# Kernel optimization log

Measured on AMD Instinct MI355X. Metric: run time of the kernel, lower is better.

The kernel has to match this reference:

```python
import jax, jax.numpy as jnp
import numpy as np

B, N, M, F, BF = 16, 1024, 12, 64, 128
N_CONV = 3
VOCAB = 100
BN_EPS = 1e-3  # keras BatchNormalization default epsilon


def _bn(x, gamma, beta):
    # inference-mode BN with moving_mean=0, moving_var=1 (keras defaults)
    return gamma * (x * (1.0 / jnp.sqrt(1.0 + BN_EPS))) + beta


def setup_inputs() -> dict:
    key = jax.random.key(0)
    ks = jax.random.split(key, 16)
    in_fea = 2 * F + BF
    inp = {
        'atom_types': jax.random.randint(ks[0], (B, N), 0, VOCAB, dtype=jnp.int32),
        'bond_fea': jax.random.normal(ks[1], (B, N, M, BF), dtype=jnp.float32),
        'nbr_list': jax.random.randint(ks[2], (B, N, M), 0, N, dtype=jnp.int32),
        'target_index': jax.random.randint(ks[3], (B, 64), 0, N, dtype=jnp.int32),
        'emb': jax.random.normal(ks[4], (VOCAB, F), dtype=jnp.float32) * 0.05,
        'core_w': jax.random.normal(ks[5], (N_CONV, in_fea, F), dtype=jnp.float32) / np.sqrt(in_fea),
        'core_b': jnp.zeros((N_CONV, F), dtype=jnp.float32),
        'filt_w': jax.random.normal(ks[6], (N_CONV, in_fea, 1), dtype=jnp.float32) / np.sqrt(in_fea),
        'filt_b': jnp.zeros((N_CONV, 1), dtype=jnp.float32),
        'bna_g': jnp.ones((N_CONV, F), dtype=jnp.float32),
        'bna_b': jnp.zeros((N_CONV, F), dtype=jnp.float32),
        'bnb_g': jnp.ones((N_CONV, F), dtype=jnp.float32),
        'bnb_b': jnp.zeros((N_CONV, F), dtype=jnp.float32),
        'dense_w': jax.random.normal(ks[7], (F, F), dtype=jnp.float32) / np.sqrt(F),
        'dense_b': jnp.zeros((F,), dtype=jnp.float32),
    }
    return inp


def _cgcnn_layer(x, bond_fea, nbr_list, cw, cb, fw, fb, bag, bab, bbg, bbb):
    # x: (B,N,F); bond_fea: (B,N,M,BF); nbr_list: (B,N,M)
    bidx = jnp.arange(x.shape[0])[:, None, None]
    atom_nbr = x[bidx, nbr_list]                       # (B,N,M,F) gather_nd
    atom_self = jnp.broadcast_to(x[:, :, None, :], atom_nbr.shape)
    total = jnp.concatenate([atom_self, atom_nbr, bond_fea], axis=-1)  # (B,N,M,2F+BF)
    core = total @ cw + cb                             # (B,N,M,F)
    filt = total @ fw + fb                             # (B,N,M,1)
    core = _bn(core, bag, bab)
    filt = jax.nn.softmax(filt, axis=2)                # softmax over neighbors
    core = jax.nn.relu(core)
    summed = jnp.mean(filt * core, axis=2)             # (B,N,F)
    summed = _bn(summed, bbg, bbb)
    return jax.nn.relu(x + summed)


def reference(atom_types, bond_fea, nbr_list, target_index, emb, core_w, core_b,
              filt_w, filt_b, bna_g, bna_b, bnb_g, bnb_b, dense_w, dense_b):
    x = emb[atom_types]                                # (B,N,F)
    for l in range(N_CONV):
        x = _cgcnn_layer(x, bond_fea, nbr_list, core_w[l], core_b[l],
                         filt_w[l], filt_b[l], bna_g[l], bna_b[l], bnb_g[l], bnb_b[l])
    bidx = jnp.arange(x.shape[0])[:, None]
    crys = x[bidx, target_index]                       # (B,N0,F) pooling gather
    crys = jax.nn.relu(crys)
    out = jax.nn.relu(crys @ dense_w + dense_b)        # (B,N0,F)
    return out
```

## Files before the change

kernel.cpp:

```cpp
#include <hip/hip_runtime.h>
#include <hip/hip_bf16.h>


#define BB 16
#define NN 1024
#define MM 12
#define FF 64
#define S_BN 0.99950037f
#define CSTR 68

typedef __attribute__((ext_vector_type(8))) short bf16x8;
typedef __attribute__((ext_vector_type(4))) float f32x4;

static __device__ __forceinline__ unsigned short f2bf(float f) {
    union { float f; unsigned u; } c; c.f = f;
    unsigned r = c.u + 0x7fff + ((c.u >> 16) & 1);
    return (unsigned short)(r >> 16);
}
static __device__ __forceinline__ float bf2f(unsigned short s) {
    union { unsigned u; float f; } c; c.u = ((unsigned)s) << 16;
    return c.f;
}
__host__ __device__ __forceinline__ int fofg(int g) { return (g & 3) * 16 + (g >> 2); }

__global__ void fold_w(const float* __restrict__ cw, const float* __restrict__ cb,
                       const float* __restrict__ g_,  const float* __restrict__ bab,
                       float* __restrict__ cwp, float* __restrict__ cbp) {
    int i = blockIdx.x * 256 + threadIdx.x;
    if (i >= 3 * 128 * 64) return;
    int g = i & 63;
    int r = (i >> 6) & 127;
    int l = i / (128 * 64);
    int f = fofg(g);
    int k = (r < 64) ? fofg(r) : 64 + fofg(r & 63);
    float gs = g_[l * 64 + f] * S_BN;
    cwp[i] = cw[(l * 256 + k) * 64 + f] * gs;
    if (r == 0)
        cbp[l * 64 + g] = cb[l * 64 + f] * gs + bab[l * 64 + f];
}

__global__ void prep_wT2(const float* __restrict__ cw, const float* __restrict__ g_,
                         const float* __restrict__ fw, unsigned short* __restrict__ wT2) {
    int i = blockIdx.x * 256 + threadIdx.x;
    if (i >= 30720) return;
    int j = i & 7;
    int t = i >> 3;
    int lane = t & 63;  t >>= 6;
    int ct = t % 5;     t /= 5;
    int kc = t & 3;
    int l  = t >> 2;
    int col = ct * 16 + (lane & 15);
    int k   = kc * 32 + (lane >> 4) * 8 + j;
    float v = 0.f;
    if (col < 64)       v = cw[(l * 256 + 128 + k) * 64 + col] * g_[l * 64 + col] * S_BN;
    else if (col == 64) v = fw[l * 256 + 128 + k];
    wT2[i] = f2bf(v);
}

__global__ void embed_k(const int* __restrict__ at, const float* __restrict__ emb,
                        float* __restrict__ x) {
    int i = blockIdx.x * 256 + threadIdx.x;
    int g = i & 63;
    int bn = i >> 6;
    x[i] = emb[at[bn] * FF + fofg(g)];
}

__global__ __launch_bounds__(256) void atomproj(
    const float* __restrict__ x, const float* __restrict__ cwp_l,
    const float* __restrict__ cbp_l, const float* __restrict__ fw_l,
    const float* __restrict__ fb_l,
    float* __restrict__ ys, float* __restrict__ yn,
    float* __restrict__ fs, float* __restrict__ fn) {
    __shared__ float wsh[128 * 64];
    __shared__ float xs[4][64];
    int tid = threadIdx.x, w = tid >> 6, lane = tid & 63;
    #pragma unroll
    for (int i = 0; i < 8; i++)
        ((float4*)wsh)[tid + 256 * i] = ((const float4*)cwp_l)[tid + 256 * i];
    int kl = fofg(lane);
    float fw1 = fw_l[kl], fw2 = fw_l[64 + kl];
    float cbv = cbp_l[lane], fbv = fb_l[0];
    __syncthreads();
    #pragma unroll 1
    for (int it = 0; it < 4; it++) {
        int row = (blockIdx.x * 4 + it) * 4 + w;
        float xl = x[(size_t)row * 64 + lane];
        xs[w][lane] = xl;
        float a1 = cbv, a2 = 0.f;
        #pragma unroll 16
        for (int k = 0; k < 64; k++) {
            float xv = xs[w][k];
            a1 += xv * wsh[k * 64 + lane];
            a2 += xv * wsh[(64 + k) * 64 + lane];
        }
        ys[(size_t)row * 64 + lane] = a1;
        yn[(size_t)row * 64 + lane] = a2;
        float p1 = xl * fw1, p2 = xl * fw2;
        #pragma unroll
        for (int off = 32; off; off >>= 1) {
            p1 += __shfl_xor(p1, off, 64);
            p2 += __shfl_xor(p2, off, 64);
        }
        if (lane == 0) { fs[row] = p1 + fbv; fn[row] = p2; }
    }
}

__global__ __launch_bounds__(256) void conv_fused(
    const float* __restrict__ bond, const unsigned short* __restrict__ wTl,
    const int* __restrict__ nbr, const float* __restrict__ x,
    const float* __restrict__ ys, const float* __restrict__ yn,
    const float* __restrict__ fs, const float* __restrict__ fn,
    const float* __restrict__ bbg, const float* __restrict__ bbb,
    float* __restrict__ xout) {
    __shared__ unsigned short csh[4][48 * CSTR];
    __shared__ float fltw[4][48];
    int tid = threadIdx.x, w = tid >> 6, lane = tid & 63;
    int mcol = lane & 15, q = lane >> 4;

    bf16x8 bw[4][5];
    #pragma unroll
    for (int kc = 0; kc < 4; kc++)
        #pragma unroll
        for (int ct = 0; ct < 5; ct++)
            bw[kc][ct] = *(const bf16x8*)(wTl + ((kc * 5 + ct) * 64 + lane) * 8);

    int rowbase = blockIdx.x * 192 + w * 48;

    #pragma unroll
    for (int rt = 0; rt < 3; rt++) {
        bf16x8 af[4];
        const float* ap0 = bond + (size_t)(rowbase + rt * 16 + mcol) * 128 + q * 8;
        #pragma unroll
        for (int kc = 0; kc < 4; kc++) {
            float4 v0 = *(const float4*)(ap0 + kc * 32);
            float4 v1 = *(const float4*)(ap0 + kc * 32 + 4);
            bf16x8 a;
            a[0] = (short)f2bf(v0.x); a[1] = (short)f2bf(v0.y);
            a[2] = (short)f2bf(v0.z); a[3] = (short)f2bf(v0.w);
            a[4] = (short)f2bf(v1.x); a[5] = (short)f2bf(v1.y);
            a[6] = (short)f2bf(v1.z); a[7] = (short)f2bf(v1.w);
            af[kc] = a;
        }
        f32x4 acc[5];
        #pragma unroll
        for (int ct = 0; ct < 5; ct++) acc[ct] = (f32x4){0.f, 0.f, 0.f, 0.f};
        #pragma unroll
        for (int kc = 0; kc < 4; kc++)
            #pragma unroll
            for (int ct = 0; ct < 5; ct++)
                acc[ct] = __builtin_amdgcn_mfma_f32_16x16x32_bf16(
                    af[kc], bw[kc][ct], acc[ct], 0, 0, 0);

        #pragma unroll
        for (int r = 0; r < 4; r++) {
            int row = rt * 16 + q * 4 + r;
            ushort4 h;
            h.x = f2bf(acc[0][r]); h.y = f2bf(acc[1][r]);
            h.z = f2bf(acc[2][r]); h.w = f2bf(acc[3][r]);
            *(ushort4*)&csh[w][row * CSTR + mcol * 4] = h;
            if (mcol == 0) fltw[w][row] = acc[4][r];
        }
    }

    int atom = blockIdx.x * 16 + w * 4 + q;
    int base = (atom >> 10) << 10;
    size_t rb = (size_t)atom * MM;
    int jv[MM];
    #pragma unroll
    for (int m = 0; m < MM; m++) jv[m] = nbr[rb + m];
    float lg[MM];
    float fsv = fs[atom];
    #pragma unroll
    for (int m = 0; m < MM; m++)
        lg[m] = fltw[w][q * MM + m] + fsv + fn[base + jv[m]];
    float mx = -1e30f;
    #pragma unroll
    for (int m = 0; m < MM; m++) mx = fmaxf(mx, lg[m]);
    float sme = 0.f;
    #pragma unroll
    for (int m = 0; m < MM; m++) { lg[m] = __expf(lg[m] - mx); sme += lg[m]; }
    float inv = 1.f / (12.f * sme);

    float4 ysv = *(const float4*)(ys + (size_t)atom * 64 + mcol * 4);
    float sum0 = 0.f, sum1 = 0.f, sum2 = 0.f, sum3 = 0.f;
    #pragma unroll
    for (int m = 0; m < MM; m++) {
        ushort4 ch = *(const ushort4*)&csh[w][(q * MM + m) * CSTR + mcol * 4];
        float4 ynv = *(const float4*)(yn + (size_t)(base + jv[m]) * 64 + mcol * 4);
        sum0 += lg[m] * fmaxf(bf2f(ch.x) + ysv.x + ynv.x, 0.f);
        sum1 += lg[m] * fmaxf(bf2f(ch.y) + ysv.y + ynv.y, 0.f);
        sum2 += lg[m] * fmaxf(bf2f(ch.z) + ysv.z + ynv.z, 0.f);
        sum3 += lg[m] * fmaxf(bf2f(ch.w) + ysv.w + ynv.w, 0.f);
    }
    float4 xv = *(const float4*)(x + (size_t)atom * 64 + mcol * 4);
    float4 o;
    o.x = fmaxf(xv.x + bbg[mcol]      * (sum0 * inv * S_BN) + bbb[mcol],      0.f);
    o.y = fmaxf(xv.y + bbg[16 + mcol] * (sum1 * inv * S_BN) + bbb[16 + mcol], 0.f);
    o.z = fmaxf(xv.z + bbg[32 + mcol] * (sum2 * inv * S_BN) + bbb[32 + mcol], 0.f);
    o.w = fmaxf(xv.w + bbg[48 + mcol] * (sum3 * inv * S_BN) + bbb[48 + mcol], 0.f);
    *(float4*)(xout + (size_t)atom * 64 + mcol * 4) = o;
}

__global__ __launch_bounds__(256) void final_k(
    const float* __restrict__ x, const int* __restrict__ tidx,
    const float* __restrict__ dw, const float* __restrict__ db,
    float* __restrict__ out) {
    __shared__ float xs[4][64];
    __shared__ float wsh[64 * 64];
    int tid = threadIdx.x;
    int w = tid >> 6, lane = tid & 63;
    const float4* src = (const float4*)dw;
    float4* dst = (float4*)wsh;
    #pragma unroll
    for (int i = 0; i < 4; i++) dst[tid + 256 * i] = src[tid + 256 * i];
    int row = blockIdx.x * 4 + w;
    int b = row >> 6;
    int t = tidx[row];
    float xv = x[((size_t)b * NN + t) * 64 + lane];
    xs[w][lane] = fmaxf(xv, 0.f);
    __syncthreads();
    float a = db[lane];
    #pragma unroll
    for (int g = 0; g < 64; g++)
        a += xs[w][g] * wsh[fofg(g) * 64 + lane];
    out[row * 64 + lane] = fmaxf(a, 0.f);
}

extern "C" void kernel_launch(void* const* d_in, const int* in_sizes, int n_in,
                              void* d_out, int out_size, void* d_ws, size_t ws_size,
                              hipStream_t stream) {
    const int*   at   = (const int*)d_in[0];
    const float* bond = (const float*)d_in[1];
    const int*   nbr  = (const int*)d_in[2];
    const int*   tgt  = (const int*)d_in[3];
    const float* emb  = (const float*)d_in[4];
    const float* cw   = (const float*)d_in[5];
    const float* cb   = (const float*)d_in[6];
    const float* fw   = (const float*)d_in[7];
    const float* fb   = (const float*)d_in[8];
    const float* bag  = (const float*)d_in[9];
    const float* bab  = (const float*)d_in[10];
    const float* bbg  = (const float*)d_in[11];
    const float* bbb  = (const float*)d_in[12];
    const float* dw   = (const float*)d_in[13];
    const float* db   = (const float*)d_in[14];

    float* ws  = (float*)d_ws;
    float* xA  = ws;
    float* xB  = xA + (size_t)BB * NN * FF;
    float* cwp = xB + (size_t)BB * NN * FF;
    float* cbp = cwp + 3 * 128 * 64;
    float* ys  = cbp + 192;
    float* yn  = ys + (size_t)BB * NN * FF;
    float* fs  = yn + (size_t)BB * NN * FF;
    float* fn  = fs + (size_t)BB * NN;
    unsigned short* wT2 = (unsigned short*)(fn + (size_t)BB * NN);

    fold_w<<<96, 256, 0, stream>>>(cw, cb, bag, bab, cwp, cbp);
    prep_wT2<<<120, 256, 0, stream>>>(cw, bag, fw, wT2);
    embed_k<<<(BB * NN * FF) / 256, 256, 0, stream>>>(at, emb, xA);

    float* xin = xA;
    float* xout = xB;
    for (int l = 0; l < 3; l++) {
        atomproj<<<BB * NN / 16, 256, 0, stream>>>(
            xin, cwp + (size_t)l * 128 * 64, cbp + l * 64, fw + l * 256, fb + l,
            ys, yn, fs, fn);
        conv_fused<<<BB * NN / 16, 256, 0, stream>>>(
            bond, wT2 + (size_t)l * 10240, nbr, xin,
            ys, yn, fs, fn, bbg + l * 64, bbb + l * 64, xout);
        float* t = xin; xin = xout; xout = t;
    }

    final_k<<<BB * 64 / 4, 256, 0, stream>>>(xin, tgt, dw, db, (float*)d_out);
}
```

Measured before the change: 295.4 us.

## Pre-convert bond features to bf16 MFMA layout once and double up conv work per wave

A new prep kernel converts the fp32 bond tensor once into bf16, laid out in MFMA fragment order. The three conv layers then read half the bytes and skip the per-layer conversion. conv_fused now stages the weight fragments in shared memory instead of registers and handles two atom tiles per wave on a 512-block grid. Loads for the second tile are issued early so they overlap the first tile's compute. This trades an extra workspace buffer, one extra kernel launch and higher register pressure from the prefetched fragments for less global traffic.

```diff
diff --git a/kernel.cpp b/kernel.cpp
--- a/kernel.cpp
+++ b/kernel.cpp
@@ -8,6 +8,7 @@
 #define FF 64
 #define S_BN 0.99950037f
 #define CSTR 68
+#define NT16 12288
 
 typedef __attribute__((ext_vector_type(8))) short bf16x8;
 typedef __attribute__((ext_vector_type(4))) float f32x4;
@@ -22,6 +23,25 @@
     return c.f;
 }
 __host__ __device__ __forceinline__ int fofg(int g) { return (g & 3) * 16 + (g >> 2); }
+
+__global__ __launch_bounds__(256) void prep_bond(const float* __restrict__ bond,
+                                                 unsigned short* __restrict__ bondf) {
+    int i = blockIdx.x * 256 + threadIdx.x;
+    int lane = i & 63;
+    int t = i >> 6;
+    int kc = t & 3;
+    int t16 = t >> 2;
+    const float* src = bond + (size_t)(t16 * 16 + (lane & 15)) * 128
+                     + kc * 32 + (lane >> 4) * 8;
+    float4 v0 = *(const float4*)src;
+    float4 v1 = *(const float4*)(src + 4);
+    uint4 o;
+    o.x = (unsigned)f2bf(v0.x) | ((unsigned)f2bf(v0.y) << 16);
+    o.y = (unsigned)f2bf(v0.z) | ((unsigned)f2bf(v0.w) << 16);
+    o.z = (unsigned)f2bf(v1.x) | ((unsigned)f2bf(v1.y) << 16);
+    o.w = (unsigned)f2bf(v1.z) | ((unsigned)f2bf(v1.w) << 16);
+    *(uint4*)(bondf + (size_t)i * 8) = o;
+}
 
 __global__ void fold_w(const float* __restrict__ cw, const float* __restrict__ cb,
                        const float* __restrict__ g_,  const float* __restrict__ bab,
@@ -106,41 +126,57 @@
 }
 
 __global__ __launch_bounds__(256) void conv_fused(
-    const float* __restrict__ bond, const unsigned short* __restrict__ wTl,
+    const unsigned short* __restrict__ bondf, const unsigned short* __restrict__ wTl,
     const int* __restrict__ nbr, const float* __restrict__ x,
     const float* __restrict__ ys, const float* __restrict__ yn,
     const float* __restrict__ fs, const float* __restrict__ fn,
     const float* __restrict__ bbg, const float* __restrict__ bbb,
     float* __restrict__ xout) {
+    __shared__ unsigned short bsh[4 * 5 * 64 * 8];
     __shared__ unsigned short csh[4][48 * CSTR];
     __shared__ float fltw[4][48];
     int tid = threadIdx.x, w = tid >> 6, lane = tid & 63;
     int mcol = lane & 15, q = lane >> 4;
 
-    bf16x8 bw[4][5];
-    #pragma unroll
-    for (int kc = 0; kc < 4; kc++)
-        #pragma unroll
-        for (int ct = 0; ct < 5; ct++)
-            bw[kc][ct] = *(const bf16x8*)(wTl + ((kc * 5 + ct) * 64 + lane) * 8);
-
-    int rowbase = blockIdx.x * 192 + w * 48;
+    #pragma unroll
+    for (int i = 0; i < 5; i++)
+        ((float4*)bsh)[tid + 256 * i] = ((const float4*)wTl)[tid + 256 * i];
+    __syncthreads();
+
+    int gw = blockIdx.x * 4 + w;
+    int wt0 = gw, wt1 = gw + 2048;
+    int a0 = wt0 * 4 + q, a1 = wt1 * 4 + q;
+    int b0 = (a0 >> 10) << 10, b1 = (a1 >> 10) << 10;
+
+    int jv0[MM], jv1[MM];
+    #pragma unroll
+    for (int m = 0; m < MM; m++) jv0[m] = nbr[(size_t)a0 * MM + m];
+    #pragma unroll
+    for (int m = 0; m < MM; m++) jv1[m] = nbr[(size_t)a1 * MM + m];
+
+    bf16x8 A0[3][4], A1[3][4];
+    #pragma unroll
+    for (int rt = 0; rt < 3; rt++)
+        #pragma unroll
+        for (int kc = 0; kc < 4; kc++)
+            A0[rt][kc] = *(const bf16x8*)(bondf +
+                (((size_t)(wt0 * 3 + rt) * 4 + kc) * 64 + lane) * 8);
+    #pragma unroll
+    for (int rt = 0; rt < 3; rt++)
+        #pragma unroll
+        for (int kc = 0; kc < 4; kc++)
+            A1[rt][kc] = *(const bf16x8*)(bondf +
+                (((size_t)(wt1 * 3 + rt) * 4 + kc) * 64 + lane) * 8);
+
+    float fnv0[MM];
+    #pragma unroll
+    for (int m = 0; m < MM; m++) fnv0[m] = fn[b0 + jv0[m]];
+    float fsv0 = fs[a0];
+    float4 ysv0 = *(const float4*)(ys + (size_t)a0 * 64 + mcol * 4);
+    float4 xv0  = *(const float4*)(x  + (size_t)a0 * 64 + mcol * 4);
 
     #pragma unroll
     for (int rt = 0; rt < 3; rt++) {
-        bf16x8 af[4];
-        const float* ap0 = bond + (size_t)(rowbase + rt * 16 + mcol) * 128 + q * 8;
-        #pragma unroll
-        for (int kc = 0; kc < 4; kc++) {
-            float4 v0 = *(const float4*)(ap0 + kc * 32);
-            float4 v1 = *(const float4*)(ap0 + kc * 32 + 4);
-            bf16x8 a;
-            a[0] = (short)f2bf(v0.x); a[1] = (short)f2bf(v0.y);
-            a[2] = (short)f2bf(v0.z); a[3] = (short)f2bf(v0.w);
-            a[4] = (short)f2bf(v1.x); a[5] = (short)f2bf(v1.y);
-            a[6] = (short)f2bf(v1.z); a[7] = (short)f2bf(v1.w);
-            af[kc] = a;
-        }
         f32x4 acc[5];
         #pragma unroll
         for (int ct = 0; ct < 5; ct++) acc[ct] = (f32x4){0.f, 0.f, 0.f, 0.f};
@@ -149,8 +185,8 @@
             #pragma unroll
             for (int ct = 0; ct < 5; ct++)
                 acc[ct] = __builtin_amdgcn_mfma_f32_16x16x32_bf16(
-                    af[kc], bw[kc][ct], acc[ct], 0, 0, 0);
-
+                    A0[rt][kc], *(const bf16x8*)&bsh[((kc * 5 + ct) * 64 + lane) * 8],
+                    acc[ct], 0, 0, 0);
         #pragma unroll
         for (int r = 0; r < 4; r++) {
             int row = rt * 16 + q * 4 + r;
@@ -162,43 +198,93 @@
         }
     }
 
-    int atom = blockIdx.x * 16 + w * 4 + q;
-    int base = (atom >> 10) << 10;
-    size_t rb = (size_t)atom * MM;
-    int jv[MM];
-    #pragma unroll
-    for (int m = 0; m < MM; m++) jv[m] = nbr[rb + m];
-    float lg[MM];
-    float fsv = fs[atom];
-    #pragma unroll
-    for (int m = 0; m < MM; m++)
-        lg[m] = fltw[w][q * MM + m] + fsv + fn[base + jv[m]];
-    float mx = -1e30f;
-    #pragma unroll
-    for (int m = 0; m < MM; m++) mx = fmaxf(mx, lg[m]);
-    float sme = 0.f;
-    #pragma unroll
-    for (int m = 0; m < MM; m++) { lg[m] = __expf(lg[m] - mx); sme += lg[m]; }
-    float inv = 1.f / (12.f * sme);
-
-    float4 ysv = *(const float4*)(ys + (size_t)atom * 64 + mcol * 4);
-    float sum0 = 0.f, sum1 = 0.f, sum2 = 0.f, sum3 = 0.f;
-    #pragma unroll
-    for (int m = 0; m < MM; m++) {
-        ushort4 ch = *(const ushort4*)&csh[w][(q * MM + m) * CSTR + mcol * 4];
-        float4 ynv = *(const float4*)(yn + (size_t)(base + jv[m]) * 64 + mcol * 4);
-        sum0 += lg[m] * fmaxf(bf2f(ch.x) + ysv.x + ynv.x, 0.f);
-        sum1 += lg[m] * fmaxf(bf2f(ch.y) + ysv.y + ynv.y, 0.f);
-        sum2 += lg[m] * fmaxf(bf2f(ch.z) + ysv.z + ynv.z, 0.f);
-        sum3 += lg[m] * fmaxf(bf2f(ch.w) + ysv.w + ynv.w, 0.f);
-    }
-    float4 xv = *(const float4*)(x + (size_t)atom * 64 + mcol * 4);
-    float4 o;
-    o.x = fmaxf(xv.x + bbg[mcol]      * (sum0 * inv * S_BN) + bbb[mcol],      0.f);
-    o.y = fmaxf(xv.y + bbg[16 + mcol] * (sum1 * inv * S_BN) + bbb[16 + mcol], 0.f);
-    o.z = fmaxf(xv.z + bbg[32 + mcol] * (sum2 * inv * S_BN) + bbb[32 + mcol], 0.f);
-    o.w = fmaxf(xv.w + bbg[48 + mcol] * (sum3 * inv * S_BN) + bbb[48 + mcol], 0.f);
-    *(float4*)(xout + (size_t)atom * 64 + mcol * 4) = o;
+    float fnv1[MM];
+    #pragma unroll
+    for (int m = 0; m < MM; m++) fnv1[m] = fn[b1 + jv1[m]];
+    float fsv1 = fs[a1];
+    float4 ysv1 = *(const float4*)(ys + (size_t)a1 * 64 + mcol * 4);
+    float4 xv1  = *(const float4*)(x  + (size_t)a1 * 64 + mcol * 4);
+
+    {
+        float lg[MM];
+        #pragma unroll
+        for (int m = 0; m < MM; m++) lg[m] = fltw[w][q * MM + m] + fsv0 + fnv0[m];
+        float mx = -1e30f;
+        #pragma unroll
+        for (int m = 0; m < MM; m++) mx = fmaxf(mx, lg[m]);
+        float sme = 0.f;
+        #pragma unroll
+        for (int m = 0; m < MM; m++) { lg[m] = __expf(lg[m] - mx); sme += lg[m]; }
+        float inv = 1.f / (12.f * sme);
+        float s0 = 0.f, s1 = 0.f, s2 = 0.f, s3 = 0.f;
+        #pragma unroll
+        for (int m = 0; m < MM; m++) {
+            ushort4 ch = *(const ushort4*)&csh[w][(q * MM + m) * CSTR + mcol * 4];
+            float4 yv = *(const float4*)(yn + (size_t)(b0 + jv0[m]) * 64 + mcol * 4);
+            s0 += lg[m] * fmaxf(bf2f(ch.x) + ysv0.x + yv.x, 0.f);
+            s1 += lg[m] * fmaxf(bf2f(ch.y) + ysv0.y + yv.y, 0.f);
+            s2 += lg[m] * fmaxf(bf2f(ch.z) + ysv0.z + yv.z, 0.f);
+            s3 += lg[m] * fmaxf(bf2f(ch.w) + ysv0.w + yv.w, 0.f);
+        }
+        float4 o;
+        o.x = fmaxf(xv0.x + bbg[mcol]      * (s0 * inv * S_BN) + bbb[mcol],      0.f);
+        o.y = fmaxf(xv0.y + bbg[16 + mcol] * (s1 * inv * S_BN) + bbb[16 + mcol], 0.f);
+        o.z = fmaxf(xv0.z + bbg[32 + mcol] * (s2 * inv * S_BN) + bbb[32 + mcol], 0.f);
+        o.w = fmaxf(xv0.w + bbg[48 + mcol] * (s3 * inv * S_BN) + bbb[48 + mcol], 0.f);
+        *(float4*)(xout + (size_t)a0 * 64 + mcol * 4) = o;
+    }
+
+    #pragma unroll
+    for (int rt = 0; rt < 3; rt++) {
+        f32x4 acc[5];
+        #pragma unroll
+        for (int ct = 0; ct < 5; ct++) acc[ct] = (f32x4){0.f, 0.f, 0.f, 0.f};
+        #pragma unroll
+        for (int kc = 0; kc < 4; kc++)
+            #pragma unroll
+            for (int ct = 0; ct < 5; ct++)
+                acc[ct] = __builtin_amdgcn_mfma_f32_16x16x32_bf16(
+                    A1[rt][kc], *(const bf16x8*)&bsh[((kc * 5 + ct) * 64 + lane) * 8],
+                    acc[ct], 0, 0, 0);
+        #pragma unroll
+        for (int r = 0; r < 4; r++) {
+            int row = rt * 16 + q * 4 + r;
+            ushort4 h;
+            h.x = f2bf(acc[0][r]); h.y = f2bf(acc[1][r]);
+            h.z = f2bf(acc[2][r]); h.w = f2bf(acc[3][r]);
+            *(ushort4*)&csh[w][row * CSTR + mcol * 4] = h;
+            if (mcol == 0) fltw[w][row] = acc[4][r];
+        }
+    }
+
+    {
+        float lg[MM];
+        #pragma unroll
+        for (int m = 0; m < MM; m++) lg[m] = fltw[w][q * MM + m] + fsv1 + fnv1[m];
+        float mx = -1e30f;
+        #pragma unroll
+        for (int m = 0; m < MM; m++) mx = fmaxf(mx, lg[m]);
+        float sme = 0.f;
+        #pragma unroll
+        for (int m = 0; m < MM; m++) { lg[m] = __expf(lg[m] - mx); sme += lg[m]; }
+        float inv = 1.f / (12.f * sme);
+        float s0 = 0.f, s1 = 0.f, s2 = 0.f, s3 = 0.f;
+        #pragma unroll
+        for (int m = 0; m < MM; m++) {
+            ushort4 ch = *(const ushort4*)&csh[w][(q * MM + m) * CSTR + mcol * 4];
+            float4 yv = *(const float4*)(yn + (size_t)(b1 + jv1[m]) * 64 + mcol * 4);
+            s0 += lg[m] * fmaxf(bf2f(ch.x) + ysv1.x + yv.x, 0.f);
+            s1 += lg[m] * fmaxf(bf2f(ch.y) + ysv1.y + yv.y, 0.f);
+            s2 += lg[m] * fmaxf(bf2f(ch.z) + ysv1.z + yv.z, 0.f);
+            s3 += lg[m] * fmaxf(bf2f(ch.w) + ysv1.w + yv.w, 0.f);
+        }
+        float4 o;
+        o.x = fmaxf(xv1.x + bbg[mcol]      * (s0 * inv * S_BN) + bbb[mcol],      0.f);
+        o.y = fmaxf(xv1.y + bbg[16 + mcol] * (s1 * inv * S_BN) + bbb[16 + mcol], 0.f);
+        o.z = fmaxf(xv1.z + bbg[32 + mcol] * (s2 * inv * S_BN) + bbb[32 + mcol], 0.f);
+        o.w = fmaxf(xv1.w + bbg[48 + mcol] * (s3 * inv * S_BN) + bbb[48 + mcol], 0.f);
+        *(float4*)(xout + (size_t)a1 * 64 + mcol * 4) = o;
+    }
 }
 
 __global__ __launch_bounds__(256) void final_k(
@@ -254,8 +340,10 @@
     float* yn  = ys + (size_t)BB * NN * FF;
     float* fs  = yn + (size_t)BB * NN * FF;
     float* fn  = fs + (size_t)BB * NN;
-    unsigned short* wT2 = (unsigned short*)(fn + (size_t)BB * NN);
-
+    unsigned short* wT2   = (unsigned short*)(fn + (size_t)BB * NN);
+    unsigned short* bondf = wT2 + 30720;
+
+    prep_bond<<<NT16, 256, 0, stream>>>(bond, bondf);
     fold_w<<<96, 256, 0, stream>>>(cw, cb, bag, bab, cwp, cbp);
     prep_wT2<<<120, 256, 0, stream>>>(cw, bag, fw, wT2);
     embed_k<<<(BB * NN * FF) / 256, 256, 0, stream>>>(at, emb, xA);
@@ -266,8 +354,8 @@
         atomproj<<<BB * NN / 16, 256, 0, stream>>>(
             xin, cwp + (size_t)l * 128 * 64, cbp + l * 64, fw + l * 256, fb + l,
             ys, yn, fs, fn);
-        conv_fused<<<BB * NN / 16, 256, 0, stream>>>(
-            bond, wT2 + (size_t)l * 10240, nbr, xin,
+        conv_fused<<<512, 256, 0, stream>>>(
+            bondf, wT2 + (size_t)l * 10240, nbr, xin,
             ys, yn, fs, fn, bbg + l * 64, bbb + l * 64, xout);
         float* t = xin; xin = xout; xout = t;
     }
```

Result: no change. 300.3 us (+1.6%).
